# Kernel optimization log

Hardware: AMD Instinct MI355X
Metric: run time of the kernel (lower is better)

Reference implementation:

```python
import jax, jax.numpy as jnp
import numpy as np

N_NODES = 100000
N_EDGES = 1000000
N_FEAT = 136
HIDDEN = 64
N_CLASSES = 2
NUM_GRAPHS = 512


def setup_inputs() -> dict:
    key = jax.random.key(0)
    ks = jax.random.split(key, 8)
    x = jax.random.normal(ks[0], (N_NODES, N_FEAT), dtype=jnp.float32)
    edge_index = jax.random.randint(ks[1], (2, N_EDGES), 0, N_NODES, dtype=jnp.int64)
    batch = jnp.sort(jax.random.randint(ks[2], (N_NODES,), 0, NUM_GRAPHS, dtype=jnp.int64))
    W1 = jax.random.normal(ks[3], (N_FEAT, HIDDEN), dtype=jnp.float32) * (1.0 / np.sqrt(N_FEAT))
    b1 = jnp.zeros((HIDDEN,), dtype=jnp.float32)
    W2 = jax.random.normal(ks[4], (HIDDEN, HIDDEN), dtype=jnp.float32) * (1.0 / np.sqrt(HIDDEN))
    b2 = jnp.zeros((HIDDEN,), dtype=jnp.float32)
    Wout = jax.random.normal(ks[5], (HIDDEN, N_CLASSES), dtype=jnp.float32) * (1.0 / np.sqrt(HIDDEN))
    bout = jnp.zeros((N_CLASSES,), dtype=jnp.float32)
    return {"x": x, "edge_index": edge_index, "batch": batch,
            "W1": W1, "b1": b1, "W2": W2, "b2": b2, "Wout": Wout, "bout": bout}


def _gcn_conv(x, src, dst, W, b, n_nodes):
    # GCNConv: D^{-1/2} (A+I) D^{-1/2} X W + b (self-loops already appended in src/dst)
    h = x @ W                                           # [N, out]
    ones = jnp.ones(src.shape, dtype=h.dtype)
    deg = jax.ops.segment_sum(ones, dst, num_segments=n_nodes)  # in-degree incl. self-loop
    dinv = jnp.where(deg > 0, jax.lax.rsqrt(deg), 0.0)
    norm = dinv[src] * dinv[dst]                        # [E]
    msg = h[src] * norm[:, None]                        # gather + normalize
    out = jax.ops.segment_sum(msg, dst, num_segments=n_nodes)   # scatter-add
    return out + b


def reference(x, edge_index, batch, W1, b1, W2, b2, Wout, bout):
    n = x.shape[0]
    loops = jnp.arange(n, dtype=edge_index.dtype)
    src = jnp.concatenate([edge_index[0], loops])
    dst = jnp.concatenate([edge_index[1], loops])

    h = jax.nn.relu(_gcn_conv(x, src, dst, W1, b1, n))
    # dropout p=0.5 is identity in eval mode
    h = jax.nn.relu(_gcn_conv(h, src, dst, W2, b2, n))

    # global_mean_pool over batch segments
    sums = jax.ops.segment_sum(h, batch, num_segments=NUM_GRAPHS)       # [G, H]
    counts = jax.ops.segment_sum(jnp.ones((n,), h.dtype), batch, num_segments=NUM_GRAPHS)
    pooled = sums / jnp.maximum(counts, 1.0)[:, None]

    return pooled @ Wout + bout                                         # [G, C]
```

## Files before the change

### kernel.cpp

```cpp
#include <hip/hip_runtime.h>
#include <hip/hip_bf16.h>

#define N_NODES   100000
#define N_EDGES   1000000
#define N_FEAT    136
#define HIDDEN    64
#define N_CLASSES 2
#define NUM_GRAPHS 512

#define NP_PAD    100352
#define SCAN_BLKS 98

#define E_PAD     1000064

#define K1_4 (N_FEAT / 4)
#define K2_4 (HIDDEN / 4)

#define K1PAD 160
#define K2PAD 72

#define NB_E    ((N_EDGES + 255) / 256)
#define NB_SC   ((N_EDGES / 4 + 255) / 256)
#define NB_HIST (NB_E + 3)
#define NB_MM   ((N_NODES + 63) / 64)
#define FUSED_GRID 5474

typedef unsigned short ushort_t;
typedef __attribute__((ext_vector_type(8))) short bf16x8;
typedef __attribute__((ext_vector_type(4))) float f32x4;
typedef __attribute__((ext_vector_type(4))) int i32x4;
typedef __attribute__((ext_vector_type(4))) unsigned short u16x4;

__device__ __forceinline__ ushort_t f2b(float v) {
    unsigned b = __float_as_uint(v);
    return (ushort_t)((b + 0x7FFF + ((b >> 16) & 1)) >> 16);
}
__device__ __forceinline__ float b2f(ushort_t u) {
    return __uint_as_float(((unsigned)u) << 16);
}
__device__ __forceinline__ unsigned pack2(float a, float b) {
    return (unsigned)f2b(a) | ((unsigned)f2b(b) << 16);
}

__global__ __launch_bounds__(256) void fused_hist_mm1_kernel(
        const int* __restrict__ dst, int* __restrict__ cnt,
        ushort_t* __restrict__ rank,
        const int* __restrict__ batch, int* __restrict__ gstart,
        const float* __restrict__ x, const float* __restrict__ W1,
        ushort_t* __restrict__ tpb) {
    __shared__ ushort_t wtb[64 * K1PAD];
    int t = threadIdx.x;
    int gq = blockIdx.x / 7, gr = blockIdx.x % 7;

    if (gr >= 2) {
        int hb = gq * 5 + (gr - 2);
        if (hb >= NB_HIST) return;
        if (hb >= NB_E) {
            int g = (hb - NB_E) * 256 + t;
            if (g <= NUM_GRAPHS) {
                int lo = 0, hi = N_NODES;
                while (lo < hi) {
                    int mid = (lo + hi) >> 1;
                    if (batch[mid] < g) lo = mid + 1; else hi = mid;
                }
                gstart[g] = lo;
            }
            return;
        }
        int e = hb * 256 + t;
        if (e < N_EDGES) {
            int d = __builtin_nontemporal_load(&dst[e]);
            int r = atomicAdd(&cnt[d], 1);
            __builtin_nontemporal_store((ushort_t)r, &rank[e]);
        }
        return;
    }

    int mb = gq * 2 + gr;
    if (mb >= NB_MM) return;
    int n0 = mb * 64;
    {
        for (int i = t; i < N_FEAT * HIDDEN; i += 256) {
            int n = i & 63, k = i >> 6;
            wtb[n * K1PAD + k] = f2b(W1[i]);
        }
        for (int i = t; i < 64 * 12; i += 256) {
            int n = i / 12, c = i % 12;
            *(unsigned*)&wtb[n * K1PAD + N_FEAT + 2 * c] = 0;
        }
    }
    __syncthreads();
    int w = t >> 6, lane = t & 63;
    int quad = lane >> 4, l16 = lane & 15;
    int an = n0 + w * 16 + l16; if (an >= N_NODES) an = N_NODES - 1;
    const f32x4* xr = (const f32x4*)(x + (long long)an * N_FEAT);
    f32x4 acc[4] = {{0,0,0,0},{0,0,0,0},{0,0,0,0},{0,0,0,0}};
#pragma unroll
    for (int kc = 0; kc < K1PAD / 32; ++kc) {
        int k0 = kc * 32 + quad * 8;
        bf16x8 a = {0, 0, 0, 0, 0, 0, 0, 0};
        if (k0 < N_FEAT) {
            f32x4 u0 = __builtin_nontemporal_load(&xr[kc * 8 + quad * 2]);
            f32x4 u1 = __builtin_nontemporal_load(&xr[kc * 8 + quad * 2 + 1]);
            union { bf16x8 v; unsigned u[4]; } cv;
            cv.u[0] = pack2(u0.x, u0.y);
            cv.u[1] = pack2(u0.z, u0.w);
            cv.u[2] = pack2(u1.x, u1.y);
            cv.u[3] = pack2(u1.z, u1.w);
            a = cv.v;
        }
#pragma unroll
        for (int nt = 0; nt < 4; ++nt) {
            bf16x8 b = *(const bf16x8*)&wtb[(nt * 16 + l16) * K1PAD + kc * 32 + quad * 8];
            acc[nt] = __builtin_amdgcn_mfma_f32_16x16x32_bf16(a, b, acc[nt], 0, 0, 0);
        }
    }
#pragma unroll
    for (int r = 0; r < 4; ++r) {
        int nl = w * 16 + quad * 4 + r;
        int node = n0 + nl;
        if (node < N_NODES) {
#pragma unroll
            for (int nt = 0; nt < 4; ++nt)
                tpb[node * 64 + nt * 16 + l16] = f2b(acc[nt][r]);
        }
    }
}

__global__ __launch_bounds__(256) void scan1_kernel(const int* __restrict__ cnt,
                                                    int* __restrict__ row_ptr,
                                                    int* __restrict__ partials) {
    __shared__ int sd[256];
    int b = blockIdx.x, t = threadIdx.x;
    int i0 = b * 1024 + t * 4;
    int c0 = (i0 + 0 < N_NODES) ? cnt[i0 + 0] : 0;
    int c1 = (i0 + 1 < N_NODES) ? cnt[i0 + 1] : 0;
    int c2 = (i0 + 2 < N_NODES) ? cnt[i0 + 2] : 0;
    int c3 = (i0 + 3 < N_NODES) ? cnt[i0 + 3] : 0;
    int tsum = c0 + c1 + c2 + c3;
    sd[t] = tsum;
    __syncthreads();
    for (int off = 1; off < 256; off <<= 1) {
        int v = (t >= off) ? sd[t - off] : 0;
        __syncthreads();
        sd[t] += v;
        __syncthreads();
    }
    int excl = sd[t] - tsum;
    row_ptr[i0 + 0] = excl;
    row_ptr[i0 + 1] = excl + c0;
    row_ptr[i0 + 2] = excl + c0 + c1;
    row_ptr[i0 + 3] = excl + c0 + c1 + c2;
    if (t == 255) partials[b] = sd[255];
}

__global__ __launch_bounds__(128) void scan2_kernel(int* __restrict__ partials) {
    __shared__ int sd[128];
    int t = threadIdx.x;
    int v = (t < SCAN_BLKS) ? partials[t] : 0;
    sd[t] = v;
    __syncthreads();
    for (int off = 1; off < 128; off <<= 1) {
        int u = (t >= off) ? sd[t - off] : 0;
        __syncthreads();
        sd[t] += u;
        __syncthreads();
    }
    partials[t] = sd[t] - v;
}

__global__ __launch_bounds__(256) void scan3_kernel(int* __restrict__ row_ptr,
                                                    const int* __restrict__ cnt,
                                                    const int* __restrict__ partials,
                                                    float* __restrict__ dinv) {
    int i = blockIdx.x * 256 + threadIdx.x;
    if (i < N_NODES) {
        int v = row_ptr[i] + partials[i >> 10];
        row_ptr[i] = v;
        dinv[i] = rsqrtf((float)(cnt[i] + 1));
    }
    if (i == N_NODES) row_ptr[N_NODES] = N_EDGES;
}

__global__ __launch_bounds__(256) void scatter_kernel(const int* __restrict__ src,
                                                      const int* __restrict__ dst,
                                                      const ushort_t* __restrict__ rank,
                                                      const int* __restrict__ row_ptr,
                                                      int* __restrict__ csr_src) {
    int e0 = (blockIdx.x * 256 + threadIdx.x) * 4;
    if (e0 >= N_EDGES) return;
    i32x4 s4 = __builtin_nontemporal_load((const i32x4*)&src[e0]);
    i32x4 d4 = __builtin_nontemporal_load((const i32x4*)&dst[e0]);
    u16x4 r4 = *(const u16x4*)&rank[e0];
    int p0 = row_ptr[d4.x] + (int)r4.x;
    int p1 = row_ptr[d4.y] + (int)r4.y;
    int p2 = row_ptr[d4.z] + (int)r4.z;
    int p3 = row_ptr[d4.w] + (int)r4.w;
    csr_src[p0] = s4.x;
    csr_src[p1] = s4.y;
    csr_src[p2] = s4.z;
    csr_src[p3] = s4.w;
}

__global__ __launch_bounds__(256) void mm2agg_kernel(
        const int* __restrict__ row_ptr, const int* __restrict__ csr_src,
        const ushort_t* __restrict__ tpb,
        const float* __restrict__ dinv,
        const float* __restrict__ W2, const float* __restrict__ bias,
        ushort_t* __restrict__ tpb2) {
    __shared__ ushort_t hsb[64 * K2PAD];
    __shared__ ushort_t wtb[64 * K2PAD];
    int t = threadIdx.x;
    int n0 = blockIdx.x * 64;
    for (int i = t; i < HIDDEN * HIDDEN; i += 256) {
        int n = i & 63, k = i >> 6;
        wtb[n * K2PAD + k] = f2b(W2[i]);
    }
    for (int i = t; i < 64 * 4; i += 256) {
        int n = i / 4, c = i % 4;
        *(unsigned*)&wtb[n * K2PAD + HIDDEN + 2 * c] = 0;
        *(unsigned*)&hsb[n * K2PAD + HIDDEN + 2 * c] = 0;
    }
    int w = t >> 6, lane = t & 63;
    float bl = bias[lane];
    for (int nl = 0; nl < 16; ++nl) {
        int n_raw = n0 + w * 16 + nl;
        int n = (n_raw < N_NODES) ? n_raw : N_NODES - 1;
        int r0 = row_ptr[n], r1 = row_ptr[n + 1];
        float a = 0.0f;
        for (int base = r0; base < r1; base += 64) {
            int cnt = r1 - base; if (cnt > 64) cnt = 64;
            int sv = csr_src[base + (lane < cnt ? lane : cnt - 1)];
            int j = 0;
            for (; j + 1 < cnt; j += 2) {
                int s0 = __builtin_amdgcn_readlane(sv, j);
                int s1 = __builtin_amdgcn_readlane(sv, j + 1);
                float v0 = dinv[s0] * b2f(tpb[(size_t)s0 * 64 + lane]);
                float v1 = dinv[s1] * b2f(tpb[(size_t)s1 * 64 + lane]);
                a += v0 + v1;
            }
            if (j < cnt) {
                int s0 = __builtin_amdgcn_readlane(sv, j);
                a += dinv[s0] * b2f(tpb[(size_t)s0 * 64 + lane]);
            }
        }
        float dn = dinv[n];
        float h = fmaxf(fmaf(fmaf(dn, b2f(tpb[(size_t)n * 64 + lane]), a), dn, bl), 0.f);
        hsb[(w * 16 + nl) * K2PAD + lane] = f2b(h);
    }
    __syncthreads();
    int quad = lane >> 4, l16 = lane & 15;
    f32x4 acc[4] = {{0,0,0,0},{0,0,0,0},{0,0,0,0},{0,0,0,0}};
#pragma unroll
    for (int kc = 0; kc < 2; ++kc) {
        bf16x8 a = *(const bf16x8*)&hsb[(w * 16 + l16) * K2PAD + kc * 32 + quad * 8];
#pragma unroll
        for (int nt = 0; nt < 4; ++nt) {
            bf16x8 b = *(const bf16x8*)&wtb[(nt * 16 + l16) * K2PAD + kc * 32 + quad * 8];
            acc[nt] = __builtin_amdgcn_mfma_f32_16x16x32_bf16(a, b, acc[nt], 0, 0, 0);
        }
    }
#pragma unroll
    for (int r = 0; r < 4; ++r) {
        int nl = w * 16 + quad * 4 + r;
        int node = n0 + nl;
        if (node < N_NODES) {
            float di = dinv[node];
#pragma unroll
            for (int nt = 0; nt < 4; ++nt)
                tpb2[node * 64 + nt * 16 + l16] = f2b(acc[nt][r] * di);
        }
    }
}

__global__ __launch_bounds__(256) void agg2_kernel(
        const int* __restrict__ row_ptr, const int* __restrict__ csr_src,
        const ushort_t* __restrict__ tpb2, const float* __restrict__ dinv,
        const float* __restrict__ bias, ushort_t* __restrict__ h2) {
    int t = threadIdx.x;
    int n0 = blockIdx.x * 64;
    int w = t >> 6, lane = t & 63;
    float bl = bias[lane];
    for (int nl = 0; nl < 16; ++nl) {
        int n = n0 + w * 16 + nl;
        if (n >= N_NODES) break;
        int r0 = row_ptr[n], r1 = row_ptr[n + 1];
        float a = 0.0f;
        for (int base = r0; base < r1; base += 64) {
            int cnt = r1 - base; if (cnt > 64) cnt = 64;
            int sv = csr_src[base + (lane < cnt ? lane : cnt - 1)];
            int j = 0;
            for (; j + 1 < cnt; j += 2) {
                int s0 = __builtin_amdgcn_readlane(sv, j);
                int s1 = __builtin_amdgcn_readlane(sv, j + 1);
                float v0 = b2f(tpb2[(size_t)s0 * 64 + lane]);
                float v1 = b2f(tpb2[(size_t)s1 * 64 + lane]);
                a += v0 + v1;
            }
            if (j < cnt) {
                int s0 = __builtin_amdgcn_readlane(sv, j);
                a += b2f(tpb2[(size_t)s0 * 64 + lane]);
            }
        }
        float dn = dinv[n];
        float h = fmaxf(fmaf(a + b2f(tpb2[(size_t)n * 64 + lane]), dn, bl), 0.f);
        h2[(size_t)n * 64 + lane] = f2b(h);
    }
}

__global__ __launch_bounds__(256) void gpool_kernel(const ushort_t* __restrict__ h2,
                                                    const int* __restrict__ gstart,
                                                    const float* __restrict__ Wout,
                                                    const float* __restrict__ bout,
                                                    float* __restrict__ out) {
    __shared__ float red[4][64];
    int lane = threadIdx.x & 63;
    int w = threadIdx.x >> 6;
    int g = blockIdx.x;
    int s = gstart[g], e = gstart[g + 1];
    float acc = 0.0f;
    for (int n = s + w; n < e; n += 4)
        acc += b2f(h2[(size_t)n * 64 + lane]);
    red[w][lane] = acc;
    __syncthreads();
    if (threadIdx.x < 64) {
        float tot = red[0][lane] + red[1][lane] + red[2][lane] + red[3][lane];
        float p = tot / fmaxf((float)(e - s), 1.0f);
        float c0 = p * Wout[lane * N_CLASSES + 0];
        float c1 = p * Wout[lane * N_CLASSES + 1];
#pragma unroll
        for (int off = 32; off > 0; off >>= 1) {
            c0 += __shfl_down(c0, off);
            c1 += __shfl_down(c1, off);
        }
        if (lane == 0) {
            out[g * N_CLASSES + 0] = c0 + bout[0];
            out[g * N_CLASSES + 1] = c1 + bout[1];
        }
    }
}

extern "C" void kernel_launch(void* const* d_in, const int* in_sizes, int n_in,
                              void* d_out, int out_size, void* d_ws, size_t ws_size,
                              hipStream_t stream) {
    const float* x     = (const float*)d_in[0];
    const int*   ei    = (const int*)d_in[1];
    const int*   batch = (const int*)d_in[2];
    const float* W1    = (const float*)d_in[3];
    const float* b1    = (const float*)d_in[4];
    const float* W2    = (const float*)d_in[5];
    const float* b2    = (const float*)d_in[6];
    const float* Wout  = (const float*)d_in[7];
    const float* bout  = (const float*)d_in[8];
    float* out = (float*)d_out;

    const int* src = ei;
    const int* dst = ei + N_EDGES;

    char* p = (char*)d_ws;
    int*      row_ptr   = (int*)p;      p += (NP_PAD + 256) * sizeof(int);
    int*      cnt       = (int*)p;      p += NP_PAD * sizeof(int);
    int*      partials  = (int*)p;      p += 256 * sizeof(int);
    int*      gstart    = (int*)p;      p += (NUM_GRAPHS + 64) * sizeof(int);
    int*      csr_src   = (int*)p;      p += (size_t)E_PAD * sizeof(int);
    float*    dinv      = (float*)p;    p += NP_PAD * sizeof(float);
    ushort_t* tpb       = (ushort_t*)p; p += (size_t)N_NODES * HIDDEN * sizeof(ushort_t);
    ushort_t* tpb2      = (ushort_t*)p; p += (size_t)N_NODES * HIDDEN * sizeof(ushort_t);
    ushort_t* rank16    = (ushort_t*)tpb2;
    ushort_t* h2        = tpb;

    hipMemsetAsync(cnt, 0, NP_PAD * sizeof(int), stream);
    fused_hist_mm1_kernel<<<FUSED_GRID, 256, 0, stream>>>(dst, cnt, rank16,
                                                          batch, gstart,
                                                          x, W1, tpb);
    scan1_kernel<<<SCAN_BLKS, 256, 0, stream>>>(cnt, row_ptr, partials);
    scan2_kernel<<<1, 128, 0, stream>>>(partials);
    scan3_kernel<<<NP_PAD / 256 + 1, 256, 0, stream>>>(row_ptr, cnt, partials, dinv);
    scatter_kernel<<<NB_SC, 256, 0, stream>>>(src, dst, rank16, row_ptr, csr_src);

    mm2agg_kernel<<<NB_MM, 256, 0, stream>>>(row_ptr, csr_src, tpb, dinv,
                                             W2, b1, tpb2);
    agg2_kernel<<<NB_MM, 256, 0, stream>>>(row_ptr, csr_src, tpb2, dinv, b2, h2);

    gpool_kernel<<<NUM_GRAPHS, 256, 0, stream>>>(h2, gstart, Wout, bout, out);
}
```

Baseline: 312.7 us.

## Split aggregation from MM2 and gather edges in parallel with feature-sliced waves

Result: slower. 400.2 us (+28.0%).

```diff
diff --git a/kernel.cpp b/kernel.cpp
--- a/kernel.cpp
+++ b/kernel.cpp
@@ -14,8 +14,6 @@
 #define E_PAD     1000064
 
 #define K1_4 (N_FEAT / 4)
-#define K2_4 (HIDDEN / 4)
-
 #define K1PAD 160
 #define K2PAD 72
 
@@ -24,6 +22,8 @@
 #define NB_HIST (NB_E + 3)
 #define NB_MM   ((N_NODES + 63) / 64)
 #define FUSED_GRID 5474
+
+#define GRID_G  8192
 
 typedef unsigned short ushort_t;
 typedef __attribute__((ext_vector_type(8))) short bf16x8;
@@ -202,13 +202,62 @@
     csr_src[p3] = s4.w;
 }
 
-__global__ __launch_bounds__(256) void mm2agg_kernel(
+template<bool L1>
+__global__ __launch_bounds__(256) void gather_kernel(
         const int* __restrict__ row_ptr, const int* __restrict__ csr_src,
-        const ushort_t* __restrict__ tpb,
-        const float* __restrict__ dinv,
-        const float* __restrict__ W2, const float* __restrict__ bias,
-        ushort_t* __restrict__ tpb2) {
-    __shared__ ushort_t hsb[64 * K2PAD];
+        const ushort_t* __restrict__ table, const float* __restrict__ dinv,
+        const float* __restrict__ bias, ushort_t* __restrict__ outb) {
+    int t = threadIdx.x;
+    int s = blockIdx.x & 3;
+    int wid = (blockIdx.x >> 2) * 4 + (t >> 6);
+    const int NWS = (GRID_G >> 2) * 4;
+    int lane = t & 63;
+    int e4 = lane >> 2;
+    int fq = lane & 3;
+    int fbase = s * 16 + fq * 4;
+    float4 bl = *(const float4*)&bias[fbase];
+
+    for (int n = wid; n < N_NODES; n += NWS) {
+        int r0 = row_ptr[n], r1 = row_ptr[n + 1];
+        float a0 = 0.f, a1 = 0.f, a2 = 0.f, a3 = 0.f;
+        for (int base = r0; base < r1; base += 16) {
+            int j = base + e4;
+            bool act = (j < r1);
+            int sv = csr_src[act ? j : r1 - 1];
+            if (act) {
+                uint2 tv = *(const uint2*)&table[(size_t)sv * 64 + fbase];
+                float sc = L1 ? dinv[sv] : 1.0f;
+                a0 = fmaf(sc, b2f((ushort_t)(tv.x & 0xffff)), a0);
+                a1 = fmaf(sc, b2f((ushort_t)(tv.x >> 16)),    a1);
+                a2 = fmaf(sc, b2f((ushort_t)(tv.y & 0xffff)), a2);
+                a3 = fmaf(sc, b2f((ushort_t)(tv.y >> 16)),    a3);
+            }
+        }
+#pragma unroll
+        for (int off = 4; off < 64; off <<= 1) {
+            a0 += __shfl_xor(a0, off);
+            a1 += __shfl_xor(a1, off);
+            a2 += __shfl_xor(a2, off);
+            a3 += __shfl_xor(a3, off);
+        }
+        if (e4 == 0) {
+            float dn = dinv[n];
+            uint2 tv = *(const uint2*)&table[(size_t)n * 64 + fbase];
+            float ss = L1 ? dn : 1.0f;
+            float h0 = fmaxf(fmaf(dn, fmaf(ss, b2f((ushort_t)(tv.x & 0xffff)), a0), bl.x), 0.f);
+            float h1 = fmaxf(fmaf(dn, fmaf(ss, b2f((ushort_t)(tv.x >> 16)),    a1), bl.y), 0.f);
+            float h2 = fmaxf(fmaf(dn, fmaf(ss, b2f((ushort_t)(tv.y & 0xffff)), a2), bl.z), 0.f);
+            float h3 = fmaxf(fmaf(dn, fmaf(ss, b2f((ushort_t)(tv.y >> 16)),    a3), bl.w), 0.f);
+            *(uint2*)&outb[(size_t)n * 64 + fbase] =
+                make_uint2(pack2(h0, h1), pack2(h2, h3));
+        }
+    }
+}
+
+__global__ __launch_bounds__(256) void mm2_kernel(const ushort_t* __restrict__ h1,
+                                                  const float* __restrict__ W2,
+                                                  const float* __restrict__ dinv,
+                                                  ushort_t* __restrict__ tpb2) {
     __shared__ ushort_t wtb[64 * K2PAD];
     int t = threadIdx.x;
     int n0 = blockIdx.x * 64;
@@ -219,41 +268,15 @@
     for (int i = t; i < 64 * 4; i += 256) {
         int n = i / 4, c = i % 4;
         *(unsigned*)&wtb[n * K2PAD + HIDDEN + 2 * c] = 0;
-        *(unsigned*)&hsb[n * K2PAD + HIDDEN + 2 * c] = 0;
-    }
+    }
+    __syncthreads();
     int w = t >> 6, lane = t & 63;
-    float bl = bias[lane];
-    for (int nl = 0; nl < 16; ++nl) {
-        int n_raw = n0 + w * 16 + nl;
-        int n = (n_raw < N_NODES) ? n_raw : N_NODES - 1;
-        int r0 = row_ptr[n], r1 = row_ptr[n + 1];
-        float a = 0.0f;
-        for (int base = r0; base < r1; base += 64) {
-            int cnt = r1 - base; if (cnt > 64) cnt = 64;
-            int sv = csr_src[base + (lane < cnt ? lane : cnt - 1)];
-            int j = 0;
-            for (; j + 1 < cnt; j += 2) {
-                int s0 = __builtin_amdgcn_readlane(sv, j);
-                int s1 = __builtin_amdgcn_readlane(sv, j + 1);
-                float v0 = dinv[s0] * b2f(tpb[(size_t)s0 * 64 + lane]);
-                float v1 = dinv[s1] * b2f(tpb[(size_t)s1 * 64 + lane]);
-                a += v0 + v1;
-            }
-            if (j < cnt) {
-                int s0 = __builtin_amdgcn_readlane(sv, j);
-                a += dinv[s0] * b2f(tpb[(size_t)s0 * 64 + lane]);
-            }
-        }
-        float dn = dinv[n];
-        float h = fmaxf(fmaf(fmaf(dn, b2f(tpb[(size_t)n * 64 + lane]), a), dn, bl), 0.f);
-        hsb[(w * 16 + nl) * K2PAD + lane] = f2b(h);
-    }
-    __syncthreads();
     int quad = lane >> 4, l16 = lane & 15;
+    int an = n0 + w * 16 + l16; if (an >= N_NODES) an = N_NODES - 1;
     f32x4 acc[4] = {{0,0,0,0},{0,0,0,0},{0,0,0,0},{0,0,0,0}};
 #pragma unroll
     for (int kc = 0; kc < 2; ++kc) {
-        bf16x8 a = *(const bf16x8*)&hsb[(w * 16 + l16) * K2PAD + kc * 32 + quad * 8];
+        bf16x8 a = *(const bf16x8*)&h1[(size_t)an * 64 + kc * 32 + quad * 8];
 #pragma unroll
         for (int nt = 0; nt < 4; ++nt) {
             bf16x8 b = *(const bf16x8*)&wtb[(nt * 16 + l16) * K2PAD + kc * 32 + quad * 8];
@@ -270,41 +293,6 @@
             for (int nt = 0; nt < 4; ++nt)
                 tpb2[node * 64 + nt * 16 + l16] = f2b(acc[nt][r] * di);
         }
-    }
-}
-
-__global__ __launch_bounds__(256) void agg2_kernel(
-        const int* __restrict__ row_ptr, const int* __restrict__ csr_src,
-        const ushort_t* __restrict__ tpb2, const float* __restrict__ dinv,
-        const float* __restrict__ bias, ushort_t* __restrict__ h2) {
-    int t = threadIdx.x;
-    int n0 = blockIdx.x * 64;
-    int w = t >> 6, lane = t & 63;
-    float bl = bias[lane];
-    for (int nl = 0; nl < 16; ++nl) {
-        int n = n0 + w * 16 + nl;
-        if (n >= N_NODES) break;
-        int r0 = row_ptr[n], r1 = row_ptr[n + 1];
-        float a = 0.0f;
-        for (int base = r0; base < r1; base += 64) {
-            int cnt = r1 - base; if (cnt > 64) cnt = 64;
-            int sv = csr_src[base + (lane < cnt ? lane : cnt - 1)];
-            int j = 0;
-            for (; j + 1 < cnt; j += 2) {
-                int s0 = __builtin_amdgcn_readlane(sv, j);
-                int s1 = __builtin_amdgcn_readlane(sv, j + 1);
-                float v0 = b2f(tpb2[(size_t)s0 * 64 + lane]);
-                float v1 = b2f(tpb2[(size_t)s1 * 64 + lane]);
-                a += v0 + v1;
-            }
-            if (j < cnt) {
-                int s0 = __builtin_amdgcn_readlane(sv, j);
-                a += b2f(tpb2[(size_t)s0 * 64 + lane]);
-            }
-        }
-        float dn = dinv[n];
-        float h = fmaxf(fmaf(a + b2f(tpb2[(size_t)n * 64 + lane]), dn, bl), 0.f);
-        h2[(size_t)n * 64 + lane] = f2b(h);
     }
 }
 
@@ -365,6 +353,7 @@
     int*      csr_src   = (int*)p;      p += (size_t)E_PAD * sizeof(int);
     float*    dinv      = (float*)p;    p += NP_PAD * sizeof(float);
     ushort_t* tpb       = (ushort_t*)p; p += (size_t)N_NODES * HIDDEN * sizeof(ushort_t);
+    ushort_t* h1        = (ushort_t*)p; p += (size_t)N_NODES * HIDDEN * sizeof(ushort_t);
     ushort_t* tpb2      = (ushort_t*)p; p += (size_t)N_NODES * HIDDEN * sizeof(ushort_t);
     ushort_t* rank16    = (ushort_t*)tpb2;
     ushort_t* h2        = tpb;
@@ -378,9 +367,12 @@
     scan3_kernel<<<NP_PAD / 256 + 1, 256, 0, stream>>>(row_ptr, cnt, partials, dinv);
     scatter_kernel<<<NB_SC, 256, 0, stream>>>(src, dst, rank16, row_ptr, csr_src);
 
-    mm2agg_kernel<<<NB_MM, 256, 0, stream>>>(row_ptr, csr_src, tpb, dinv,
-                                             W2, b1, tpb2);
-    agg2_kernel<<<NB_MM, 256, 0, stream>>>(row_ptr, csr_src, tpb2, dinv, b2, h2);
+    gather_kernel<true><<<GRID_G, 256, 0, stream>>>(row_ptr, csr_src, tpb,
+                                                    dinv, b1, h1);
+    mm2_kernel<<<NB_MM, 256, 0, stream>>>(h1, W2, dinv, tpb2);
+
+    gather_kernel<false><<<GRID_G, 256, 0, stream>>>(row_ptr, csr_src, tpb2,
+                                                     dinv, b2, h2);
 
     gpool_kernel<<<NUM_GRAPHS, 256, 0, stream>>>(h2, gstart, Wout, bout, out);
 }
```
